# Performance work log

Measured on AMD Instinct MI355X. Metric: run time of the kernel, lower is better.

Reference implementation:

```python
import jax, jax.numpy as jnp
import numpy as np

EPS = 1e-6
HIDDEN = 8
SCALE = 1.0 / HIDDEN ** 0.5


def l2_normalize(t, axis=-1, eps=EPS):
    return t * jax.lax.rsqrt(jnp.sum(jnp.square(t), axis=axis, keepdims=True) + eps)


def setup_inputs() -> dict:
    key = jax.random.key(0)
    ks = jax.random.split(key, 6)
    B, S, N, D_IN, D_OUT = 2, 4096, 8, 2048, 2048
    x = jax.random.normal(ks[0], (B, S, D_IN), dtype=jnp.float32)
    bax = jax.random.normal(ks[1], (B, S, N, D_OUT), dtype=jnp.float32)
    # Linear params (stored as [in, hidden] for x @ W + b)
    W_q = jax.random.normal(ks[2], (D_IN, HIDDEN), dtype=jnp.float32) / np.sqrt(D_IN)
    b_q = jax.random.normal(ks[3], (HIDDEN,), dtype=jnp.float32) * 0.01
    W_k = jax.random.normal(ks[4], (D_OUT, HIDDEN), dtype=jnp.float32) / np.sqrt(D_OUT)
    b_k = jax.random.normal(ks[5], (HIDDEN,), dtype=jnp.float32) * 0.01
    return {"x": x, "bax": bax, "W_q": W_q, "b_q": b_q, "W_k": W_k, "b_k": b_k}


def reference(x, bax, W_q, b_q, W_k, b_k):
    # L2 normalize over feature dim
    xn = l2_normalize(x)                     # [B, S, D_in]
    baxn = l2_normalize(bax)                 # [B, S, N, D_out]
    queries = xn @ W_q + b_q                 # [B, S, H]
    keys = baxn @ W_k + b_k                  # [B, S, N, H]
    # scores: contract hidden dim per (b, s) position
    scores = jnp.einsum('bsh,bsnh->bsn', queries, keys) * SCALE  # [B, S, N]
    attention = jax.nn.softmax(scores, axis=-1)
    return attention
```

## Files before the change

kernel.cpp:

```cpp
#include <hip/hip_runtime.h>
#include <cstdint>

#define DIN 2048
#define ROWS 9
#define SCALE_F 0.35355339059327373f
#define EPS_F 1e-6f

__global__ __launch_bounds__(512, 4)
void router_kernel(const float* __restrict__ x, const float* __restrict__ bax,
                   const float* __restrict__ Wq, const float* __restrict__ bq,
                   const float* __restrict__ Wk, const float* __restrict__ bk,
                   float* __restrict__ out, int positions) {
    __shared__ float red[2][ROWS][8][9];
    __shared__ float ssb[2][ROWS][8];

    const int t = threadIdx.x;
    const int w = t >> 6;
    const int lane = t & 63;
    const int kn = lane >> 3;
    const int hh = lane & 7;

    float wq[32], wk[32];
    {
        const float4* q4 = (const float4*)(Wq + 32 * t);
        const float4* k4 = (const float4*)(Wk + 32 * t);
#pragma unroll
        for (int j = 0; j < 8; ++j) {
            float4 a = q4[j];
            wq[4 * j + 0] = a.x; wq[4 * j + 1] = a.y;
            wq[4 * j + 2] = a.z; wq[4 * j + 3] = a.w;
        }
#pragma unroll
        for (int j = 0; j < 8; ++j) {
            float4 b = k4[j];
            wk[4 * j + 0] = b.x; wk[4 * j + 1] = b.y;
            wk[4 * j + 2] = b.z; wk[4 * j + 3] = b.w;
        }
    }
    const float kbias = bk[hh];
    const float qbias = bq[hh];

    const int stride = gridDim.x;
    int buf = 0;
    for (long p = blockIdx.x; p < positions; p += stride, buf ^= 1) {
        const float4* xr = (const float4*)(x + p * (long)DIN) + t;
        const float4* br = (const float4*)(bax + p * (long)(8 * DIN)) + t;

        float4 v[ROWS];
#pragma unroll
        for (int r = 0; r < 5; ++r)
            v[r] = (r == 0) ? xr[0] : br[(r - 1) * (DIN / 4)];

        float ssv[ROWS];
#pragma unroll
        for (int r = 0; r < ROWS; ++r) {
            if (r < 4) v[r + 5] = br[(r + 4) * (DIN / 4)];

            float e[4] = { v[r].x, v[r].y, v[r].z, v[r].w };
            ssv[r] = fmaf(e[3], e[3], fmaf(e[2], e[2], fmaf(e[1], e[1], e[0] * e[0])));

            const float* wa = (r == 0) ? wq : wk;
            float pd[8];
#pragma unroll
            for (int h = 0; h < 8; ++h)
                pd[h] = fmaf(e[3], wa[24 + h],
                         fmaf(e[2], wa[16 + h],
                          fmaf(e[1], wa[8 + h], e[0] * wa[h])));

            float r1[4];
#pragma unroll
            for (int i = 0; i < 4; ++i) {
                float keep = (lane & 1) ? pd[i + 4] : pd[i];
                float send = (lane & 1) ? pd[i] : pd[i + 4];
                r1[i] = keep + __shfl_xor(send, 1);
            }
            float r2[2];
#pragma unroll
            for (int i = 0; i < 2; ++i) {
                float keep = (lane & 2) ? r1[i + 2] : r1[i];
                float send = (lane & 2) ? r1[i] : r1[i + 2];
                r2[i] = keep + __shfl_xor(send, 2);
            }
            float keep = (lane & 4) ? r2[1] : r2[0];
            float send = (lane & 4) ? r2[0] : r2[1];
            float dv = keep + __shfl_xor(send, 4);
            dv += __shfl_xor(dv, 8);
            dv += __shfl_xor(dv, 16);
            dv += __shfl_xor(dv, 32);
            if (lane < 8)
                red[buf][r][w][((lane & 1) << 2) | (lane & 2) | ((lane & 4) >> 2)] = dv;
        }

        {
            float r1[4];
#pragma unroll
            for (int i = 0; i < 4; ++i) {
                float keep = (lane & 1) ? ssv[i + 4] : ssv[i];
                float send = (lane & 1) ? ssv[i] : ssv[i + 4];
                r1[i] = keep + __shfl_xor(send, 1);
            }
            float r2[2];
#pragma unroll
            for (int i = 0; i < 2; ++i) {
                float keep = (lane & 2) ? r1[i + 2] : r1[i];
                float send = (lane & 2) ? r1[i] : r1[i + 2];
                r2[i] = keep + __shfl_xor(send, 2);
            }
            float keep = (lane & 4) ? r2[1] : r2[0];
            float send = (lane & 4) ? r2[0] : r2[1];
            float sv = keep + __shfl_xor(send, 4);
            sv += __shfl_xor(sv, 8);
            sv += __shfl_xor(sv, 16);
            sv += __shfl_xor(sv, 32);
            if (lane < 8)
                ssb[buf][((lane & 1) << 2) | (lane & 2) | ((lane & 4) >> 2)][w] = sv;
            float s8 = ssv[8];
#pragma unroll
            for (int m = 1; m < 64; m <<= 1) s8 += __shfl_xor(s8, m);
            if (lane == 0) ssb[buf][8][w] = s8;
        }

        __syncthreads();

        if (w == 0) {
            float dtk = 0.f, ssk = 0.f, dtq = 0.f, ssq = 0.f;
#pragma unroll
            for (int wv = 0; wv < 8; ++wv) {
                dtk += red[buf][kn + 1][wv][hh];
                ssk += ssb[buf][kn + 1][wv];
                dtq += red[buf][0][wv][hh];
                ssq += ssb[buf][0][wv];
            }
            float kval = fmaf(dtk, rsqrtf(ssk + EPS_F), kbias);
            float qval = fmaf(dtq, rsqrtf(ssq + EPS_F), qbias);
            float s = qval * kval;
            s += __shfl_xor(s, 1);
            s += __shfl_xor(s, 2);
            s += __shfl_xor(s, 4);
            s *= SCALE_F;
            float mx = s;
            mx = fmaxf(mx, __shfl_xor(mx, 8));
            mx = fmaxf(mx, __shfl_xor(mx, 16));
            mx = fmaxf(mx, __shfl_xor(mx, 32));
            float ev = __expf(s - mx);
            float den = ev;
            den += __shfl_xor(den, 8);
            den += __shfl_xor(den, 16);
            den += __shfl_xor(den, 32);
            if (hh == 0) out[p * 8 + kn] = ev / den;
        }
    }
}

extern "C" void kernel_launch(void* const* d_in, const int* in_sizes, int n_in,
                              void* d_out, int out_size, void* d_ws, size_t ws_size,
                              hipStream_t stream) {
    const float* x   = (const float*)d_in[0];
    const float* bax = (const float*)d_in[1];
    const float* Wq  = (const float*)d_in[2];
    const float* bq  = (const float*)d_in[3];
    const float* Wk  = (const float*)d_in[4];
    const float* bk  = (const float*)d_in[5];
    float* out = (float*)d_out;

    const int positions = in_sizes[0] / DIN;
    int nb = positions < 512 ? positions : 512;
    router_kernel<<<nb, 512, 0, stream>>>(x, bax, Wq, bq, Wk, bk, out, positions);
}
```

Before: 120.7 us.

## Launch one block per position instead of a persistent grid-stride loop

Replaces the persistent 512-block grid-stride loop with one block per position (8192 blocks). All nine row loads are issued up front, before the weight loads, so memory latency overlaps with loading the weights. The double-buffered shared memory goes away because each block handles a single position. In exchange, every block reloads the 32+32 weight values per thread, adding weight traffic that mostly hits cache, and pays extra block launch overhead.

Measured after the change: 191.7 us. 58.8% more time.

```diff
diff --git a/kernel.cpp b/kernel.cpp
--- a/kernel.cpp
+++ b/kernel.cpp
@@ -11,14 +11,22 @@
                    const float* __restrict__ Wq, const float* __restrict__ bq,
                    const float* __restrict__ Wk, const float* __restrict__ bk,
                    float* __restrict__ out, int positions) {
-    __shared__ float red[2][ROWS][8][9];
-    __shared__ float ssb[2][ROWS][8];
+    __shared__ float red[ROWS][8][9];
+    __shared__ float ssb[ROWS][8];
 
     const int t = threadIdx.x;
     const int w = t >> 6;
     const int lane = t & 63;
     const int kn = lane >> 3;
     const int hh = lane & 7;
+    const long p = blockIdx.x;
+
+    const float4* xr = (const float4*)(x + p * (long)DIN) + t;
+    const float4* br = (const float4*)(bax + p * (long)(8 * DIN)) + t;
+    float4 v[ROWS];
+    v[0] = xr[0];
+#pragma unroll
+    for (int r = 1; r < ROWS; ++r) v[r] = br[(r - 1) * (DIN / 4)];
 
     float wq[32], wk[32];
     {
@@ -37,118 +45,102 @@
             wk[4 * j + 2] = b.z; wk[4 * j + 3] = b.w;
         }
     }
-    const float kbias = bk[hh];
-    const float qbias = bq[hh];
 
-    const int stride = gridDim.x;
-    int buf = 0;
-    for (long p = blockIdx.x; p < positions; p += stride, buf ^= 1) {
-        const float4* xr = (const float4*)(x + p * (long)DIN) + t;
-        const float4* br = (const float4*)(bax + p * (long)(8 * DIN)) + t;
+    float ssv[ROWS];
+#pragma unroll
+    for (int r = 0; r < ROWS; ++r) {
+        float e[4] = { v[r].x, v[r].y, v[r].z, v[r].w };
+        ssv[r] = fmaf(e[3], e[3], fmaf(e[2], e[2], fmaf(e[1], e[1], e[0] * e[0])));
 
-        float4 v[ROWS];
+        const float* wa = (r == 0) ? wq : wk;
+        float pd[8];
 #pragma unroll
-        for (int r = 0; r < 5; ++r)
-            v[r] = (r == 0) ? xr[0] : br[(r - 1) * (DIN / 4)];
+        for (int h = 0; h < 8; ++h)
+            pd[h] = fmaf(e[3], wa[24 + h],
+                     fmaf(e[2], wa[16 + h],
+                      fmaf(e[1], wa[8 + h], e[0] * wa[h])));
 
-        float ssv[ROWS];
+        float r1[4];
 #pragma unroll
-        for (int r = 0; r < ROWS; ++r) {
-            if (r < 4) v[r + 5] = br[(r + 4) * (DIN / 4)];
+        for (int i = 0; i < 4; ++i) {
+            float keep = (lane & 1) ? pd[i + 4] : pd[i];
+            float send = (lane & 1) ? pd[i] : pd[i + 4];
+            r1[i] = keep + __shfl_xor(send, 1);
+        }
+        float r2[2];
+#pragma unroll
+        for (int i = 0; i < 2; ++i) {
+            float keep = (lane & 2) ? r1[i + 2] : r1[i];
+            float send = (lane & 2) ? r1[i] : r1[i + 2];
+            r2[i] = keep + __shfl_xor(send, 2);
+        }
+        float keep = (lane & 4) ? r2[1] : r2[0];
+        float send = (lane & 4) ? r2[0] : r2[1];
+        float dv = keep + __shfl_xor(send, 4);
+        dv += __shfl_xor(dv, 8);
+        dv += __shfl_xor(dv, 16);
+        dv += __shfl_xor(dv, 32);
+        if (lane < 8)
+            red[r][w][((lane & 1) << 2) | (lane & 2) | ((lane & 4) >> 2)] = dv;
+    }
 
-            float e[4] = { v[r].x, v[r].y, v[r].z, v[r].w };
-            ssv[r] = fmaf(e[3], e[3], fmaf(e[2], e[2], fmaf(e[1], e[1], e[0] * e[0])));
+    {
+        float r1[4];
+#pragma unroll
+        for (int i = 0; i < 4; ++i) {
+            float keep = (lane & 1) ? ssv[i + 4] : ssv[i];
+            float send = (lane & 1) ? ssv[i] : ssv[i + 4];
+            r1[i] = keep + __shfl_xor(send, 1);
+        }
+        float r2[2];
+#pragma unroll
+        for (int i = 0; i < 2; ++i) {
+            float keep = (lane & 2) ? r1[i + 2] : r1[i];
+            float send = (lane & 2) ? r1[i] : r1[i + 2];
+            r2[i] = keep + __shfl_xor(send, 2);
+        }
+        float keep = (lane & 4) ? r2[1] : r2[0];
+        float send = (lane & 4) ? r2[0] : r2[1];
+        float sv = keep + __shfl_xor(send, 4);
+        sv += __shfl_xor(sv, 8);
+        sv += __shfl_xor(sv, 16);
+        sv += __shfl_xor(sv, 32);
+        if (lane < 8)
+            ssb[((lane & 1) << 2) | (lane & 2) | ((lane & 4) >> 2)][w] = sv;
+        float s8 = ssv[8];
+#pragma unroll
+        for (int m = 1; m < 64; m <<= 1) s8 += __shfl_xor(s8, m);
+        if (lane == 0) ssb[8][w] = s8;
+    }
 
-            const float* wa = (r == 0) ? wq : wk;
-            float pd[8];
+    __syncthreads();
+
+    if (w == 0) {
+        float dtk = 0.f, ssk = 0.f, dtq = 0.f, ssq = 0.f;
 #pragma unroll
-            for (int h = 0; h < 8; ++h)
-                pd[h] = fmaf(e[3], wa[24 + h],
-                         fmaf(e[2], wa[16 + h],
-                          fmaf(e[1], wa[8 + h], e[0] * wa[h])));
-
-            float r1[4];
-#pragma unroll
-            for (int i = 0; i < 4; ++i) {
-                float keep = (lane & 1) ? pd[i + 4] : pd[i];
-                float send = (lane & 1) ? pd[i] : pd[i + 4];
-                r1[i] = keep + __shfl_xor(send, 1);
-            }
-            float r2[2];
-#pragma unroll
-            for (int i = 0; i < 2; ++i) {
-                float keep = (lane & 2) ? r1[i + 2] : r1[i];
-                float send = (lane & 2) ? r1[i] : r1[i + 2];
-                r2[i] = keep + __shfl_xor(send, 2);
-            }
-            float keep = (lane & 4) ? r2[1] : r2[0];
-            float send = (lane & 4) ? r2[0] : r2[1];
-            float dv = keep + __shfl_xor(send, 4);
-            dv += __shfl_xor(dv, 8);
-            dv += __shfl_xor(dv, 16);
-            dv += __shfl_xor(dv, 32);
-            if (lane < 8)
-                red[buf][r][w][((lane & 1) << 2) | (lane & 2) | ((lane & 4) >> 2)] = dv;
+        for (int wv = 0; wv < 8; ++wv) {
+            dtk += red[kn + 1][wv][hh];
+            ssk += ssb[kn + 1][wv];
+            dtq += red[0][wv][hh];
+            ssq += ssb[0][wv];
         }
-
-        {
-            float r1[4];
-#pragma unroll
-            for (int i = 0; i < 4; ++i) {
-                float keep = (lane & 1) ? ssv[i + 4] : ssv[i];
-                float send = (lane & 1) ? ssv[i] : ssv[i + 4];
-                r1[i] = keep + __shfl_xor(send, 1);
-            }
-            float r2[2];
-#pragma unroll
-            for (int i = 0; i < 2; ++i) {
-                float keep = (lane & 2) ? r1[i + 2] : r1[i];
-                float send = (lane & 2) ? r1[i] : r1[i + 2];
-                r2[i] = keep + __shfl_xor(send, 2);
-            }
-            float keep = (lane & 4) ? r2[1] : r2[0];
-            float send = (lane & 4) ? r2[0] : r2[1];
-            float sv = keep + __shfl_xor(send, 4);
-            sv += __shfl_xor(sv, 8);
-            sv += __shfl_xor(sv, 16);
-            sv += __shfl_xor(sv, 32);
-            if (lane < 8)
-                ssb[buf][((lane & 1) << 2) | (lane & 2) | ((lane & 4) >> 2)][w] = sv;
-            float s8 = ssv[8];
-#pragma unroll
-            for (int m = 1; m < 64; m <<= 1) s8 += __shfl_xor(s8, m);
-            if (lane == 0) ssb[buf][8][w] = s8;
-        }
-
-        __syncthreads();
-
-        if (w == 0) {
-            float dtk = 0.f, ssk = 0.f, dtq = 0.f, ssq = 0.f;
-#pragma unroll
-            for (int wv = 0; wv < 8; ++wv) {
-                dtk += red[buf][kn + 1][wv][hh];
-                ssk += ssb[buf][kn + 1][wv];
-                dtq += red[buf][0][wv][hh];
-                ssq += ssb[buf][0][wv];
-            }
-            float kval = fmaf(dtk, rsqrtf(ssk + EPS_F), kbias);
-            float qval = fmaf(dtq, rsqrtf(ssq + EPS_F), qbias);
-            float s = qval * kval;
-            s += __shfl_xor(s, 1);
-            s += __shfl_xor(s, 2);
-            s += __shfl_xor(s, 4);
-            s *= SCALE_F;
-            float mx = s;
-            mx = fmaxf(mx, __shfl_xor(mx, 8));
-            mx = fmaxf(mx, __shfl_xor(mx, 16));
-            mx = fmaxf(mx, __shfl_xor(mx, 32));
-            float ev = __expf(s - mx);
-            float den = ev;
-            den += __shfl_xor(den, 8);
-            den += __shfl_xor(den, 16);
-            den += __shfl_xor(den, 32);
-            if (hh == 0) out[p * 8 + kn] = ev / den;
-        }
+        float kval = fmaf(dtk, rsqrtf(ssk + EPS_F), bk[hh]);
+        float qval = fmaf(dtq, rsqrtf(ssq + EPS_F), bq[hh]);
+        float s = qval * kval;
+        s += __shfl_xor(s, 1);
+        s += __shfl_xor(s, 2);
+        s += __shfl_xor(s, 4);
+        s *= SCALE_F;
+        float mx = s;
+        mx = fmaxf(mx, __shfl_xor(mx, 8));
+        mx = fmaxf(mx, __shfl_xor(mx, 16));
+        mx = fmaxf(mx, __shfl_xor(mx, 32));
+        float ev = __expf(s - mx);
+        float den = ev;
+        den += __shfl_xor(den, 8);
+        den += __shfl_xor(den, 16);
+        den += __shfl_xor(den, 32);
+        if (hh == 0) out[p * 8 + kn] = ev / den;
     }
 }
 
@@ -164,6 +156,5 @@
     float* out = (float*)d_out;
 
     const int positions = in_sizes[0] / DIN;
-    int nb = positions < 512 ? positions : 512;
-    router_kernel<<<nb, 512, 0, stream>>>(x, bax, Wq, bq, Wk, bk, out, positions);
+    router_kernel<<<positions, 512, 0, stream>>>(x, bax, Wq, bq, Wk, bk, out, positions);
 }
```

## Prefetch next position's rows during compute and merge sum-of-squares into reduction buffer

Applied to the files above, without the earlier changes.

Loads for the next grid-stride position are issued right after each row's registers are consumed, so global loads overlap the current position's math. The sum-of-squares reduction is now a plain per-row butterfly, and its result is stored in an extra slot of the shared reduction array instead of a separate buffer. __syncthreads is replaced with an explicit lgkmcnt wait plus s_barrier, so the barrier does not wait on the outstanding prefetch loads. The extra butterfly shuffles and register pressure from holding all nine float4s across iterations may offset the gain, and the last iteration redundantly reloads the same position.

After: 213.6 us. 76.9% more time.

```diff
diff --git a/kernel.cpp b/kernel.cpp
--- a/kernel.cpp
+++ b/kernel.cpp
@@ -11,14 +11,15 @@
                    const float* __restrict__ Wq, const float* __restrict__ bq,
                    const float* __restrict__ Wk, const float* __restrict__ bk,
                    float* __restrict__ out, int positions) {
-    __shared__ float red[2][ROWS][8][9];
-    __shared__ float ssb[2][ROWS][8];
+    __shared__ float red[2][ROWS][8][13];
 
     const int t = threadIdx.x;
     const int w = t >> 6;
     const int lane = t & 63;
     const int kn = lane >> 3;
     const int hh = lane & 7;
+    const int chan = ((lane & 1) << 2) | (lane & 2) | ((lane & 4) >> 2);
+    const int widx = (lane < 8) ? chan : 8;
 
     float wq[32], wk[32];
     {
@@ -37,35 +38,43 @@
             wk[4 * j + 2] = b.z; wk[4 * j + 3] = b.w;
         }
     }
-    const float kbias = bk[hh];
-    const float qbias = bq[hh];
+    const float bkh = bk[hh];
+    const float bqh = bq[hh];
 
     const int stride = gridDim.x;
-    int buf = 0;
-    for (long p = blockIdx.x; p < positions; p += stride, buf ^= 1) {
+    long p = blockIdx.x;
+    if (p >= positions) return;
+
+    float4 v[ROWS];
+    {
         const float4* xr = (const float4*)(x + p * (long)DIN) + t;
         const float4* br = (const float4*)(bax + p * (long)(8 * DIN)) + t;
+        v[0] = xr[0];
+#pragma unroll
+        for (int r = 1; r < ROWS; ++r) v[r] = br[(r - 1) * (DIN / 4)];
+    }
 
-        float4 v[ROWS];
-#pragma unroll
-        for (int r = 0; r < 5; ++r)
-            v[r] = (r == 0) ? xr[0] : br[(r - 1) * (DIN / 4)];
+    int buf = 0;
+    for (; p < positions; p += stride, buf ^= 1) {
+        const long pn = (p + stride < positions) ? (p + stride) : p;
+        const float4* xr_n = (const float4*)(x + pn * (long)DIN) + t;
+        const float4* br_n = (const float4*)(bax + pn * (long)(8 * DIN)) + t;
 
-        float ssv[ROWS];
 #pragma unroll
         for (int r = 0; r < ROWS; ++r) {
-            if (r < 4) v[r + 5] = br[(r + 4) * (DIN / 4)];
+            const float e0 = v[r].x, e1 = v[r].y, e2 = v[r].z, e3 = v[r].w;
+            if (r == 0) v[0] = xr_n[0];
+            else        v[r] = br_n[(r - 1) * (DIN / 4)];
 
-            float e[4] = { v[r].x, v[r].y, v[r].z, v[r].w };
-            ssv[r] = fmaf(e[3], e[3], fmaf(e[2], e[2], fmaf(e[1], e[1], e[0] * e[0])));
+            float ss = fmaf(e3, e3, fmaf(e2, e2, fmaf(e1, e1, e0 * e0)));
 
             const float* wa = (r == 0) ? wq : wk;
             float pd[8];
 #pragma unroll
             for (int h = 0; h < 8; ++h)
-                pd[h] = fmaf(e[3], wa[24 + h],
-                         fmaf(e[2], wa[16 + h],
-                          fmaf(e[1], wa[8 + h], e[0] * wa[h])));
+                pd[h] = fmaf(e3, wa[24 + h],
+                         fmaf(e2, wa[16 + h],
+                          fmaf(e1, wa[8 + h], e0 * wa[h])));
 
             float r1[4];
 #pragma unroll
@@ -87,52 +96,31 @@
             dv += __shfl_xor(dv, 8);
             dv += __shfl_xor(dv, 16);
             dv += __shfl_xor(dv, 32);
-            if (lane < 8)
-                red[buf][r][w][((lane & 1) << 2) | (lane & 2) | ((lane & 4) >> 2)] = dv;
+
+            ss += __shfl_xor(ss, 1);
+            ss += __shfl_xor(ss, 2);
+            ss += __shfl_xor(ss, 4);
+            ss += __shfl_xor(ss, 8);
+            ss += __shfl_xor(ss, 16);
+            ss += __shfl_xor(ss, 32);
+
+            if (lane < 9) red[buf][r][w][widx] = (lane < 8) ? dv : ss;
         }
 
-        {
-            float r1[4];
-#pragma unroll
-            for (int i = 0; i < 4; ++i) {
-                float keep = (lane & 1) ? ssv[i + 4] : ssv[i];
-                float send = (lane & 1) ? ssv[i] : ssv[i + 4];
-                r1[i] = keep + __shfl_xor(send, 1);
-            }
-            float r2[2];
-#pragma unroll
-            for (int i = 0; i < 2; ++i) {
-                float keep = (lane & 2) ? r1[i + 2] : r1[i];
-                float send = (lane & 2) ? r1[i] : r1[i + 2];
-                r2[i] = keep + __shfl_xor(send, 2);
-            }
-            float keep = (lane & 4) ? r2[1] : r2[0];
-            float send = (lane & 4) ? r2[0] : r2[1];
-            float sv = keep + __shfl_xor(send, 4);
-            sv += __shfl_xor(sv, 8);
-            sv += __shfl_xor(sv, 16);
-            sv += __shfl_xor(sv, 32);
-            if (lane < 8)
-                ssb[buf][((lane & 1) << 2) | (lane & 2) | ((lane & 4) >> 2)][w] = sv;
-            float s8 = ssv[8];
-#pragma unroll
-            for (int m = 1; m < 64; m <<= 1) s8 += __shfl_xor(s8, m);
-            if (lane == 0) ssb[buf][8][w] = s8;
-        }
-
-        __syncthreads();
+        asm volatile("s_waitcnt lgkmcnt(0)" ::: "memory");
+        asm volatile("s_barrier" ::: "memory");
 
         if (w == 0) {
             float dtk = 0.f, ssk = 0.f, dtq = 0.f, ssq = 0.f;
 #pragma unroll
             for (int wv = 0; wv < 8; ++wv) {
                 dtk += red[buf][kn + 1][wv][hh];
-                ssk += ssb[buf][kn + 1][wv];
+                ssk += red[buf][kn + 1][wv][8];
                 dtq += red[buf][0][wv][hh];
-                ssq += ssb[buf][0][wv];
+                ssq += red[buf][0][wv][8];
             }
-            float kval = fmaf(dtk, rsqrtf(ssk + EPS_F), kbias);
-            float qval = fmaf(dtq, rsqrtf(ssq + EPS_F), qbias);
+            float kval = fmaf(dtk, rsqrtf(ssk + EPS_F), bkh);
+            float qval = fmaf(dtq, rsqrtf(ssq + EPS_F), bqh);
             float s = qval * kval;
             s += __shfl_xor(s, 1);
             s += __shfl_xor(s, 2);
```
